# Optimization experiments

Hardware: AMD Instinct MI355X
Metric: run time of the kernel (lower is better)

## Reference

```python
import jax, jax.numpy as jnp
import numpy as np
import math

B, H, T, N = 2, 16, 4096, 64  # N = mlp_internal_dim_multiplier * n_embd // n_head = 1*1024//16
THETA = 2.0 ** 16


def _cos_sin(T, N):
    # quantized-theta RoPE tables, matching get_freqs + angle construction
    t = jnp.arange(N, dtype=jnp.float32)
    tq = jnp.floor(t / 2.0) * 2.0                      # quantize(t, q=2)
    freqs = 1.0 / (THETA ** (tq / N)) / (2.0 * math.pi)  # [N]
    phases = jnp.arange(T, dtype=jnp.float32)[:, None] * freqs[None, :]  # [T,N]
    ang = (phases % 1.0) * (2.0 * math.pi)
    return jnp.cos(ang), jnp.sin(ang)                  # each [T,N]


def setup_inputs() -> dict:
    key = jax.random.key(0)
    kq, kv = jax.random.split(key)
    Q = jax.random.normal(kq, (B, H, T, N), dtype=jnp.float32)
    V = jax.random.normal(kv, (B, H, T, N), dtype=jnp.float32)
    return {"Q": Q, "V": V}


def reference(Q, V):
    # K is Q (asserted in the torch module); RoPE applied to Q only.
    b, h, t, n = Q.shape
    cos, sin = _cos_sin(t, n)                          # [t,n], broadcast over b,h
    q_rot = jnp.stack((-Q[..., 1::2], Q[..., ::2]), axis=-1).reshape(Q.shape)
    QR = Q * cos + q_rot * sin                         # [b,h,t,n]
    scores = jnp.einsum('bhtn,bhsn->bhts', QR, QR) * (n ** -0.5)
    # strict lower-triangular mask (tril with diagonal=-1): no softmax
    mask = jnp.tril(jnp.ones((t, t), dtype=bool), k=-1)
    scores = jnp.where(mask, scores, 0.0)
    return jnp.einsum('bhts,bhsn->bhtn', scores, V)
```

## Files before the change

kernel.cpp:

```cpp
#include <hip/hip_runtime.h>

#define T_SEQ 4096
#define NDIM 64
#define BH 32
#define TN (T_SEQ * NDIM)

typedef short short8 __attribute__((ext_vector_type(8)));
typedef float f32x16 __attribute__((ext_vector_type(16)));
typedef unsigned uint2e __attribute__((ext_vector_type(2)));

static __device__ __forceinline__ unsigned packbf(float lo, float hi) {
    unsigned r;
    asm("v_cvt_pk_bf16_f32 %0, %1, %2" : "=v"(r) : "v"(lo), "v"(hi));
    return r;
}
static __device__ __forceinline__ unsigned short f2bf(float x) {
    union { float f; unsigned u; } v; v.f = x;
    return (unsigned short)((v.u + 0x8000u) >> 16);
}
static __device__ __forceinline__ f32x16 mfma32(short8 a, short8 b, f32x16 c) {
    return __builtin_amdgcn_mfma_f32_32x32x16_bf16(a, b, c, 0, 0, 0);
}

static __device__ __forceinline__ void half_swap(unsigned &x, unsigned &y) {
#if __has_builtin(__builtin_amdgcn_permlane32_swap)
    uint2e r = __builtin_amdgcn_permlane32_swap(x, y, false, false);
    x = r[0]; y = r[1];
#else
    int sl = (((int)threadIdx.x & 63) ^ 32) << 2;
    unsigned bx = (unsigned)__builtin_amdgcn_ds_bpermute(sl, (int)x);
    unsigned by = (unsigned)__builtin_amdgcn_ds_bpermute(sl, (int)y);
    bool hi = (threadIdx.x & 32) != 0;
    unsigned nx = hi ? by : x;
    unsigned ny = hi ? y : bx;
    x = nx; y = ny;
#endif
}

static __device__ __forceinline__ void tile_to_frags(const f32x16 &sc, short8 &f0, short8 &f1) {
    unsigned d[4][2];
#pragma unroll
    for (int g = 0; g < 4; ++g) {
        d[g][0] = packbf(sc[4 * g + 0], sc[4 * g + 1]);
        d[g][1] = packbf(sc[4 * g + 2], sc[4 * g + 3]);
    }
    half_swap(d[0][0], d[1][0]);
    half_swap(d[0][1], d[1][1]);
    half_swap(d[2][0], d[3][0]);
    half_swap(d[2][1], d[3][1]);
    union { unsigned u[4]; short8 s; } a, b;
    a.u[0] = d[0][0]; a.u[1] = d[0][1]; a.u[2] = d[1][0]; a.u[3] = d[1][1];
    b.u[0] = d[2][0]; b.u[1] = d[2][1]; b.u[2] = d[3][0]; b.u[3] = d[3][1];
    f0 = a.s; f1 = b.s;
}

__global__ __launch_bounds__(256) void rope_kernel(const float* __restrict__ Q,
                                                   unsigned short* __restrict__ qf) {
    const int bhtb = blockIdx.x;
    const int tb = bhtb & 127;
    const int bh = bhtb >> 7;
    const int np = threadIdx.x & 31;
    const int tg = threadIdx.x >> 5;
    const float freq = exp2f(-0.5f * (float)np) * 0.15915494309189535f;
    const int kc = np >> 3, hi = (np >> 2) & 1, jw = np & 3;
    const float2* qsrc = (const float2*)(Q + ((size_t)bh * T_SEQ + tb * 32) * NDIM);
    unsigned* qdst = (unsigned*)(qf + (size_t)bh * TN + (size_t)tb * 32 * NDIM);
#pragma unroll
    for (int it = 0; it < 4; ++it) {
        const int tl = tg * 4 + it;
        const int t = tb * 32 + tl;
        float2 q = qsrc[tl * 32 + np];
        float ph = (float)t * freq;
        float ang = (ph - floorf(ph)) * 6.283185307179586f;
        float s, c;
        __sincosf(ang, &s, &c);
        float r0 = q.x * c - q.y * s;
        float r1 = q.y * c + q.x * s;
        qdst[kc * 256 + (tl * 2 + hi) * 4 + jw] = packbf(r0, r1);
    }
}

__global__ __launch_bounds__(256) void vtrans_kernel(const float* __restrict__ V,
                                                     unsigned short* __restrict__ vfr) {
    __shared__ float tile[128 * 65];
    const int sb = blockIdx.x;
    const int bh = blockIdx.y;
    const int tid = threadIdx.x;
    const float* vsrc = V + ((size_t)bh * T_SEQ + sb * 128) * NDIM;
#pragma unroll
    for (int i = 0; i < 8; ++i) {
        int e = (i * 256 + tid) * 4;
        int row = e >> 6, col = e & 63;
        float4 d4 = *(const float4*)(vsrc + e);
        tile[row * 65 + col + 0] = d4.x; tile[row * 65 + col + 1] = d4.y;
        tile[row * 65 + col + 2] = d4.z; tile[row * 65 + col + 3] = d4.w;
    }
    __syncthreads();
    unsigned short* dst = vfr + (size_t)bh * TN + (size_t)sb * 8192;
#pragma unroll
    for (int u = 0; u < 4; ++u) {
        int g = u * 256 + tid;
        int kc = g >> 7, dh = g & 127;
        int d = dh >> 1, hh = dh & 1;
        int sbase = kc * 16 + hh * 8;
        uint4 o;
        o.x = packbf(tile[(sbase + 0) * 65 + d] * 0.125f, tile[(sbase + 1) * 65 + d] * 0.125f);
        o.y = packbf(tile[(sbase + 2) * 65 + d] * 0.125f, tile[(sbase + 3) * 65 + d] * 0.125f);
        o.z = packbf(tile[(sbase + 4) * 65 + d] * 0.125f, tile[(sbase + 5) * 65 + d] * 0.125f);
        o.w = packbf(tile[(sbase + 6) * 65 + d] * 0.125f, tile[(sbase + 7) * 65 + d] * 0.125f);
        *(uint4*)(dst + g * 8) = o;
    }
}

__global__ __launch_bounds__(256, 2) void attn_kernel(const unsigned short* __restrict__ qf,
                                                      const unsigned short* __restrict__ vfr,
                                                      float* __restrict__ out) {
    __shared__ float4 red[2][4][4][64];

    const int tid = threadIdx.x;
    const int lane = tid & 63;
    const int w = tid >> 6;
    const int ws = w >> 1, wt = w & 1;
    const int l31 = lane & 31, hi = lane >> 5;

    const int blk = blockIdx.x;
    const int bh = blk & 31;
    const int qb = 31 - (blk >> 5);
    const int t0 = qb * 128;

    const unsigned short* qfh = qf + (size_t)bh * TN;
    const unsigned short* vfh = vfr + (size_t)bh * TN;
    float* out_h = out + (size_t)bh * TN;

    const int lhx16 = (l31 * 2 + hi) * 8;

    short8 bq[2][4];
#pragma unroll
    for (int tt2 = 0; tt2 < 2; ++tt2) {
        const int r32 = (t0 >> 5) + 2 * wt + tt2;
#pragma unroll
        for (int kc = 0; kc < 4; ++kc)
            bq[tt2][kc] = *(const short8*)(qfh + (size_t)(r32 * 4 + kc) * 512 + lhx16);
    }

    f32x16 oacc[2][2];
#pragma unroll
    for (int a = 0; a < 2; ++a)
#pragma unroll
        for (int b = 0; b < 2; ++b)
#pragma unroll
            for (int r = 0; r < 16; ++r) oacc[a][b][r] = 0.0f;

    short8 ak[2][4];
#pragma unroll
    for (int st2 = 0; st2 < 2; ++st2) {
        const int r32 = 2 * ws + st2;
#pragma unroll
        for (int kc = 0; kc < 4; ++kc)
            ak[st2][kc] = *(const short8*)(qfh + (size_t)(r32 * 4 + kc) * 512 + lhx16);
    }

    for (int sb = 0; sb <= qb; ++sb) {
        f32x16 sacc[2][2];
#pragma unroll
        for (int a = 0; a < 2; ++a)
#pragma unroll
            for (int b = 0; b < 2; ++b)
#pragma unroll
                for (int r = 0; r < 16; ++r) sacc[a][b][r] = 0.0f;
#pragma unroll
        for (int st2 = 0; st2 < 2; ++st2)
#pragma unroll
            for (int tt2 = 0; tt2 < 2; ++tt2)
#pragma unroll
                for (int kc = 0; kc < 4; ++kc)
                    sacc[st2][tt2] = mfma32(ak[st2][kc], bq[tt2][kc], sacc[st2][tt2]);

        short8 akn[2][4];
        if (sb < qb) {
#pragma unroll
            for (int st2 = 0; st2 < 2; ++st2) {
                const int r32 = (sb + 1) * 4 + 2 * ws + st2;
#pragma unroll
                for (int kc = 0; kc < 4; ++kc)
                    akn[st2][kc] = *(const short8*)(qfh + (size_t)(r32 * 4 + kc) * 512 + lhx16);
            }
        }

        if (sb == qb) {
#pragma unroll
            for (int st2 = 0; st2 < 2; ++st2) {
                const int st = 2 * ws + st2;
#pragma unroll
                for (int tt2 = 0; tt2 < 2; ++tt2) {
                    const int tg = (2 * wt + tt2) * 32 + l31;
#pragma unroll
                    for (int r = 0; r < 16; ++r) {
                        const int sg = st * 32 + (r & 3) + 8 * (r >> 2) + 4 * hi;
                        if (sg >= tg) sacc[st2][tt2][r] = 0.0f;
                    }
                }
            }
        }

        short8 pa[2][4];
#pragma unroll
        for (int st2 = 0; st2 < 2; ++st2)
#pragma unroll
            for (int tt2 = 0; tt2 < 2; ++tt2)
                tile_to_frags(sacc[st2][tt2], pa[tt2][2 * st2 + 0], pa[tt2][2 * st2 + 1]);

#pragma unroll
        for (int kc4 = 0; kc4 < 4; ++kc4) {
            const int kcg = 4 * ws + kc4;
            short8 v0 = *(const short8*)(vfh + (size_t)sb * 8192 + (size_t)kcg * 1024 + lhx16);
            short8 v1 = *(const short8*)(vfh + (size_t)sb * 8192 + (size_t)kcg * 1024 + 512 + lhx16);
            oacc[0][0] = mfma32(pa[0][kc4], v0, oacc[0][0]);
            oacc[0][1] = mfma32(pa[0][kc4], v1, oacc[0][1]);
            oacc[1][0] = mfma32(pa[1][kc4], v0, oacc[1][0]);
            oacc[1][1] = mfma32(pa[1][kc4], v1, oacc[1][1]);
        }

        if (sb < qb) {
#pragma unroll
            for (int st2 = 0; st2 < 2; ++st2)
#pragma unroll
                for (int kc = 0; kc < 4; ++kc)
                    ak[st2][kc] = akn[st2][kc];
        }
    }

    if (ws == 1) {
#pragma unroll
        for (int tt2 = 0; tt2 < 2; ++tt2)
#pragma unroll
            for (int dd = 0; dd < 2; ++dd)
#pragma unroll
                for (int g = 0; g < 4; ++g) {
                    float4 v;
                    v.x = oacc[tt2][dd][4 * g + 0];
                    v.y = oacc[tt2][dd][4 * g + 1];
                    v.z = oacc[tt2][dd][4 * g + 2];
                    v.w = oacc[tt2][dd][4 * g + 3];
                    red[wt][tt2 * 2 + dd][g][lane] = v;
                }
    }
    __syncthreads();
    if (ws == 0) {
#pragma unroll
        for (int tt2 = 0; tt2 < 2; ++tt2)
#pragma unroll
            for (int dd = 0; dd < 2; ++dd) {
#pragma unroll
                for (int g = 0; g < 4; ++g) {
                    float4 o = red[wt][tt2 * 2 + dd][g][lane];
                    oacc[tt2][dd][4 * g + 0] += o.x;
                    oacc[tt2][dd][4 * g + 1] += o.y;
                    oacc[tt2][dd][4 * g + 2] += o.z;
                    oacc[tt2][dd][4 * g + 3] += o.w;
                }
#pragma unroll
                for (int r = 0; r < 16; ++r) {
                    const int rl = (r & 3) + 8 * (r >> 2) + 4 * hi;
                    out_h[(size_t)(t0 + 64 * wt + 32 * tt2 + rl) * NDIM + 32 * dd + l31] =
                        oacc[tt2][dd][r];
                }
            }
    }
    (void)f2bf(0.0f);
}

extern "C" void kernel_launch(void* const* d_in, const int* in_sizes, int n_in,
                              void* d_out, int out_size, void* d_ws, size_t ws_size,
                              hipStream_t stream) {
    (void)in_sizes; (void)n_in; (void)out_size; (void)ws_size;
    const float* Q = (const float*)d_in[0];
    const float* V = (const float*)d_in[1];
    float* out = (float*)d_out;

    unsigned short* qf  = (unsigned short*)d_ws;
    unsigned short* vfr = qf + (size_t)BH * TN;

    rope_kernel<<<BH * 128, 256, 0, stream>>>(Q, qf);
    vtrans_kernel<<<dim3(T_SEQ / 128, BH), 256, 0, stream>>>(V, vfr);
    attn_kernel<<<BH * 32, 256, 0, stream>>>(qf, vfr, out);
}
```

Measured before the change: 177.3 us.

## Split attention block across eight waves with per-tile diagonal skipping

Each block now runs 512 threads as eight waves. Every wave owns one 32-row query tile and half of each 128-key block, where before four waves each owned two query tiles. On the diagonal key block, waves skip key tiles that lie fully above the causal mask instead of computing and then zeroing them. The software prefetch of next-block keys is removed, and K and V fragments are loaded inline per tile. The intent is more wave parallelism, lower register pressure, higher occupancy and less wasted diagonal work, at the cost of more redundant Q/V loads per block and losing the explicit prefetch.

```diff
diff --git a/kernel.cpp b/kernel.cpp
--- a/kernel.cpp
+++ b/kernel.cpp
@@ -13,10 +13,6 @@
     unsigned r;
     asm("v_cvt_pk_bf16_f32 %0, %1, %2" : "=v"(r) : "v"(lo), "v"(hi));
     return r;
-}
-static __device__ __forceinline__ unsigned short f2bf(float x) {
-    union { float f; unsigned u; } v; v.f = x;
-    return (unsigned short)((v.u + 0x8000u) >> 16);
 }
 static __device__ __forceinline__ f32x16 mfma32(short8 a, short8 b, f32x16 c) {
     return __builtin_amdgcn_mfma_f32_32x32x16_bf16(a, b, c, 0, 0, 0);
@@ -112,15 +108,15 @@
     }
 }
 
-__global__ __launch_bounds__(256, 2) void attn_kernel(const unsigned short* __restrict__ qf,
+__global__ __launch_bounds__(512, 3) void attn_kernel(const unsigned short* __restrict__ qf,
                                                       const unsigned short* __restrict__ vfr,
                                                       float* __restrict__ out) {
-    __shared__ float4 red[2][4][4][64];
+    __shared__ float4 red[4][2][4][64];
 
     const int tid = threadIdx.x;
     const int lane = tid & 63;
     const int w = tid >> 6;
-    const int ws = w >> 1, wt = w & 1;
+    const int ws = w >> 2, wt = w & 3;
     const int l31 = lane & 31, hi = lane >> 5;
 
     const int blk = blockIdx.x;
@@ -134,140 +130,96 @@
 
     const int lhx16 = (l31 * 2 + hi) * 8;
 
-    short8 bq[2][4];
-#pragma unroll
-    for (int tt2 = 0; tt2 < 2; ++tt2) {
-        const int r32 = (t0 >> 5) + 2 * wt + tt2;
+    short8 bq[4];
+    {
+        const int tr32 = (t0 >> 5) + wt;
 #pragma unroll
         for (int kc = 0; kc < 4; ++kc)
-            bq[tt2][kc] = *(const short8*)(qfh + (size_t)(r32 * 4 + kc) * 512 + lhx16);
-    }
-
-    f32x16 oacc[2][2];
+            bq[kc] = *(const short8*)(qfh + (size_t)(tr32 * 4 + kc) * 512 + lhx16);
+    }
+
+    f32x16 oacc[2];
 #pragma unroll
     for (int a = 0; a < 2; ++a)
 #pragma unroll
-        for (int b = 0; b < 2; ++b)
-#pragma unroll
-            for (int r = 0; r < 16; ++r) oacc[a][b][r] = 0.0f;
-
-    short8 ak[2][4];
-#pragma unroll
-    for (int st2 = 0; st2 < 2; ++st2) {
-        const int r32 = 2 * ws + st2;
-#pragma unroll
-        for (int kc = 0; kc < 4; ++kc)
-            ak[st2][kc] = *(const short8*)(qfh + (size_t)(r32 * 4 + kc) * 512 + lhx16);
-    }
+        for (int r = 0; r < 16; ++r) oacc[a][r] = 0.0f;
 
     for (int sb = 0; sb <= qb; ++sb) {
-        f32x16 sacc[2][2];
-#pragma unroll
-        for (int a = 0; a < 2; ++a)
-#pragma unroll
-            for (int b = 0; b < 2; ++b)
-#pragma unroll
-                for (int r = 0; r < 16; ++r) sacc[a][b][r] = 0.0f;
-#pragma unroll
-        for (int st2 = 0; st2 < 2; ++st2)
-#pragma unroll
-            for (int tt2 = 0; tt2 < 2; ++tt2)
-#pragma unroll
-                for (int kc = 0; kc < 4; ++kc)
-                    sacc[st2][tt2] = mfma32(ak[st2][kc], bq[tt2][kc], sacc[st2][tt2]);
-
-        short8 akn[2][4];
-        if (sb < qb) {
-#pragma unroll
-            for (int st2 = 0; st2 < 2; ++st2) {
-                const int r32 = (sb + 1) * 4 + 2 * ws + st2;
-#pragma unroll
-                for (int kc = 0; kc < 4; ++kc)
-                    akn[st2][kc] = *(const short8*)(qfh + (size_t)(r32 * 4 + kc) * 512 + lhx16);
-            }
+        const bool diag = (sb == qb);
+#pragma unroll
+        for (int st2 = 0; st2 < 2; ++st2) {
+            const int idx = 2 * ws + st2;
+            if (diag && idx > wt) continue;
+
+            const int sr32 = sb * 4 + idx;
+            short8 vf00 = *(const short8*)(vfh + (size_t)sb * 8192 + (size_t)(2 * idx + 0) * 1024 + lhx16);
+            short8 vf01 = *(const short8*)(vfh + (size_t)sb * 8192 + (size_t)(2 * idx + 0) * 1024 + 512 + lhx16);
+            short8 vf10 = *(const short8*)(vfh + (size_t)sb * 8192 + (size_t)(2 * idx + 1) * 1024 + lhx16);
+            short8 vf11 = *(const short8*)(vfh + (size_t)sb * 8192 + (size_t)(2 * idx + 1) * 1024 + 512 + lhx16);
+
+            short8 ak[4];
+#pragma unroll
+            for (int kc = 0; kc < 4; ++kc)
+                ak[kc] = *(const short8*)(qfh + (size_t)(sr32 * 4 + kc) * 512 + lhx16);
+
+            f32x16 sacc;
+#pragma unroll
+            for (int r = 0; r < 16; ++r) sacc[r] = 0.0f;
+#pragma unroll
+            for (int kc = 0; kc < 4; ++kc)
+                sacc = mfma32(ak[kc], bq[kc], sacc);
+
+            if (diag && idx == wt) {
+                const int tg = l31;
+#pragma unroll
+                for (int r = 0; r < 16; ++r) {
+                    const int sg = (r & 3) + 8 * (r >> 2) + 4 * hi;
+                    if (sg >= tg) sacc[r] = 0.0f;
+                }
+            }
+
+            short8 p0, p1;
+            tile_to_frags(sacc, p0, p1);
+
+            oacc[0] = mfma32(p0, vf00, oacc[0]);
+            oacc[1] = mfma32(p0, vf01, oacc[1]);
+            oacc[0] = mfma32(p1, vf10, oacc[0]);
+            oacc[1] = mfma32(p1, vf11, oacc[1]);
         }
-
-        if (sb == qb) {
-#pragma unroll
-            for (int st2 = 0; st2 < 2; ++st2) {
-                const int st = 2 * ws + st2;
-#pragma unroll
-                for (int tt2 = 0; tt2 < 2; ++tt2) {
-                    const int tg = (2 * wt + tt2) * 32 + l31;
-#pragma unroll
-                    for (int r = 0; r < 16; ++r) {
-                        const int sg = st * 32 + (r & 3) + 8 * (r >> 2) + 4 * hi;
-                        if (sg >= tg) sacc[st2][tt2][r] = 0.0f;
-                    }
-                }
-            }
-        }
-
-        short8 pa[2][4];
-#pragma unroll
-        for (int st2 = 0; st2 < 2; ++st2)
-#pragma unroll
-            for (int tt2 = 0; tt2 < 2; ++tt2)
-                tile_to_frags(sacc[st2][tt2], pa[tt2][2 * st2 + 0], pa[tt2][2 * st2 + 1]);
-
-#pragma unroll
-        for (int kc4 = 0; kc4 < 4; ++kc4) {
-            const int kcg = 4 * ws + kc4;
-            short8 v0 = *(const short8*)(vfh + (size_t)sb * 8192 + (size_t)kcg * 1024 + lhx16);
-            short8 v1 = *(const short8*)(vfh + (size_t)sb * 8192 + (size_t)kcg * 1024 + 512 + lhx16);
-            oacc[0][0] = mfma32(pa[0][kc4], v0, oacc[0][0]);
-            oacc[0][1] = mfma32(pa[0][kc4], v1, oacc[0][1]);
-            oacc[1][0] = mfma32(pa[1][kc4], v0, oacc[1][0]);
-            oacc[1][1] = mfma32(pa[1][kc4], v1, oacc[1][1]);
-        }
-
-        if (sb < qb) {
-#pragma unroll
-            for (int st2 = 0; st2 < 2; ++st2)
-#pragma unroll
-                for (int kc = 0; kc < 4; ++kc)
-                    ak[st2][kc] = akn[st2][kc];
-        }
     }
 
     if (ws == 1) {
 #pragma unroll
-        for (int tt2 = 0; tt2 < 2; ++tt2)
-#pragma unroll
-            for (int dd = 0; dd < 2; ++dd)
-#pragma unroll
-                for (int g = 0; g < 4; ++g) {
-                    float4 v;
-                    v.x = oacc[tt2][dd][4 * g + 0];
-                    v.y = oacc[tt2][dd][4 * g + 1];
-                    v.z = oacc[tt2][dd][4 * g + 2];
-                    v.w = oacc[tt2][dd][4 * g + 3];
-                    red[wt][tt2 * 2 + dd][g][lane] = v;
-                }
+        for (int dd = 0; dd < 2; ++dd)
+#pragma unroll
+            for (int g = 0; g < 4; ++g) {
+                float4 v;
+                v.x = oacc[dd][4 * g + 0];
+                v.y = oacc[dd][4 * g + 1];
+                v.z = oacc[dd][4 * g + 2];
+                v.w = oacc[dd][4 * g + 3];
+                red[wt][dd][g][lane] = v;
+            }
     }
     __syncthreads();
     if (ws == 0) {
 #pragma unroll
-        for (int tt2 = 0; tt2 < 2; ++tt2)
-#pragma unroll
-            for (int dd = 0; dd < 2; ++dd) {
-#pragma unroll
-                for (int g = 0; g < 4; ++g) {
-                    float4 o = red[wt][tt2 * 2 + dd][g][lane];
-                    oacc[tt2][dd][4 * g + 0] += o.x;
-                    oacc[tt2][dd][4 * g + 1] += o.y;
-                    oacc[tt2][dd][4 * g + 2] += o.z;
-                    oacc[tt2][dd][4 * g + 3] += o.w;
-                }
-#pragma unroll
-                for (int r = 0; r < 16; ++r) {
-                    const int rl = (r & 3) + 8 * (r >> 2) + 4 * hi;
-                    out_h[(size_t)(t0 + 64 * wt + 32 * tt2 + rl) * NDIM + 32 * dd + l31] =
-                        oacc[tt2][dd][r];
-                }
-            }
-    }
-    (void)f2bf(0.0f);
+        for (int dd = 0; dd < 2; ++dd) {
+#pragma unroll
+            for (int g = 0; g < 4; ++g) {
+                float4 o = red[wt][dd][g][lane];
+                oacc[dd][4 * g + 0] += o.x;
+                oacc[dd][4 * g + 1] += o.y;
+                oacc[dd][4 * g + 2] += o.z;
+                oacc[dd][4 * g + 3] += o.w;
+            }
+#pragma unroll
+            for (int r = 0; r < 16; ++r) {
+                const int rl = (r & 3) + 8 * (r >> 2) + 4 * hi;
+                out_h[(size_t)(t0 + 32 * wt + rl) * NDIM + 32 * dd + l31] = oacc[dd][r];
+            }
+        }
+    }
 }
 
 extern "C" void kernel_launch(void* const* d_in, const int* in_sizes, int n_in,
@@ -283,5 +235,5 @@
 
     rope_kernel<<<BH * 128, 256, 0, stream>>>(Q, qf);
     vtrans_kernel<<<dim3(T_SEQ / 128, BH), 256, 0, stream>>>(V, vfr);
-    attn_kernel<<<BH * 32, 256, 0, stream>>>(qf, vfr, out);
-}
+    attn_kernel<<<BH * 32, 512, 0, stream>>>(qf, vfr, out);
+}
```

Result: no change. 180.8 us (+2.0%).

## Software-pipeline attention loop: overlap next S-phase MFMAs with current O-phase

Applied to the files above, without the earlier changes.

Restructures the attention main loop into a software pipeline. Iteration sb now converts scores sb to bf16 fragments, computes scores for block sb+1, runs the O-phase MFMAs for block sb, and prefetches K two blocks ahead and V one block ahead into registers. The diagonal mask now runs only once, in an epilogue after the loop. The goal is to hide global-load latency and the dependency stalls between the score MFMAs, the fragment transform and the output MFMAs, at the cost of more live registers (V fragments plus the score accumulators), which could raise spills under launch_bounds(256,2).

```diff
diff --git a/kernel.cpp b/kernel.cpp
--- a/kernel.cpp
+++ b/kernel.cpp
@@ -13,10 +13,6 @@
     unsigned r;
     asm("v_cvt_pk_bf16_f32 %0, %1, %2" : "=v"(r) : "v"(lo), "v"(hi));
     return r;
-}
-static __device__ __forceinline__ unsigned short f2bf(float x) {
-    union { float f; unsigned u; } v; v.f = x;
-    return (unsigned short)((v.u + 0x8000u) >> 16);
 }
 static __device__ __forceinline__ f32x16 mfma32(short8 a, short8 b, f32x16 c) {
     return __builtin_amdgcn_mfma_f32_32x32x16_bf16(a, b, c, 0, 0, 0);
@@ -112,6 +108,58 @@
     }
 }
 
+static __device__ __forceinline__ void load_ak4(const unsigned short* qfh, int sb, int ws,
+                                                int lhx16, short8 (&A)[2][4]) {
+    const int r32base = sb * 4 + 2 * ws;
+#pragma unroll
+    for (int st2 = 0; st2 < 2; ++st2)
+#pragma unroll
+        for (int kc = 0; kc < 4; ++kc)
+            A[st2][kc] = *(const short8*)(qfh + (size_t)((r32base + st2) * 4 + kc) * 512 + lhx16);
+}
+static __device__ __forceinline__ void load_vf8(const unsigned short* vfh, int sb, int ws,
+                                                int lhx16, short8 (&V)[4][2]) {
+#pragma unroll
+    for (int kc4 = 0; kc4 < 4; ++kc4) {
+        const size_t base = (size_t)sb * 8192 + (size_t)(4 * ws + kc4) * 1024 + lhx16;
+        V[kc4][0] = *(const short8*)(vfh + base);
+        V[kc4][1] = *(const short8*)(vfh + base + 512);
+    }
+}
+static __device__ __forceinline__ void s_phase(const short8 (&ak)[2][4], const short8 (&bq)[2][4],
+                                               f32x16 (&sacc)[2][2]) {
+#pragma unroll
+    for (int a = 0; a < 2; ++a)
+#pragma unroll
+        for (int b = 0; b < 2; ++b)
+#pragma unroll
+            for (int r = 0; r < 16; ++r) sacc[a][b][r] = 0.0f;
+#pragma unroll
+    for (int st2 = 0; st2 < 2; ++st2)
+#pragma unroll
+        for (int tt2 = 0; tt2 < 2; ++tt2)
+#pragma unroll
+            for (int kc = 0; kc < 4; ++kc)
+                sacc[st2][tt2] = mfma32(ak[st2][kc], bq[tt2][kc], sacc[st2][tt2]);
+}
+static __device__ __forceinline__ void transform_all(const f32x16 (&sacc)[2][2], short8 (&pa)[2][4]) {
+#pragma unroll
+    for (int st2 = 0; st2 < 2; ++st2)
+#pragma unroll
+        for (int tt2 = 0; tt2 < 2; ++tt2)
+            tile_to_frags(sacc[st2][tt2], pa[tt2][2 * st2 + 0], pa[tt2][2 * st2 + 1]);
+}
+static __device__ __forceinline__ void o_phase(const short8 (&pa)[2][4], const short8 (&vf)[4][2],
+                                               f32x16 (&oacc)[2][2]) {
+#pragma unroll
+    for (int kc4 = 0; kc4 < 4; ++kc4) {
+        oacc[0][0] = mfma32(pa[0][kc4], vf[kc4][0], oacc[0][0]);
+        oacc[0][1] = mfma32(pa[0][kc4], vf[kc4][1], oacc[0][1]);
+        oacc[1][0] = mfma32(pa[1][kc4], vf[kc4][0], oacc[1][0]);
+        oacc[1][1] = mfma32(pa[1][kc4], vf[kc4][1], oacc[1][1]);
+    }
+}
+
 __global__ __launch_bounds__(256, 2) void attn_kernel(const unsigned short* __restrict__ qf,
                                                       const unsigned short* __restrict__ vfr,
                                                       float* __restrict__ out) {
@@ -151,83 +199,40 @@
 #pragma unroll
             for (int r = 0; r < 16; ++r) oacc[a][b][r] = 0.0f;
 
-    short8 ak[2][4];
-#pragma unroll
-    for (int st2 = 0; st2 < 2; ++st2) {
-        const int r32 = 2 * ws + st2;
-#pragma unroll
-        for (int kc = 0; kc < 4; ++kc)
-            ak[st2][kc] = *(const short8*)(qfh + (size_t)(r32 * 4 + kc) * 512 + lhx16);
-    }
-
-    for (int sb = 0; sb <= qb; ++sb) {
-        f32x16 sacc[2][2];
-#pragma unroll
-        for (int a = 0; a < 2; ++a)
-#pragma unroll
-            for (int b = 0; b < 2; ++b)
-#pragma unroll
-                for (int r = 0; r < 16; ++r) sacc[a][b][r] = 0.0f;
-#pragma unroll
-        for (int st2 = 0; st2 < 2; ++st2)
-#pragma unroll
-            for (int tt2 = 0; tt2 < 2; ++tt2)
-#pragma unroll
-                for (int kc = 0; kc < 4; ++kc)
-                    sacc[st2][tt2] = mfma32(ak[st2][kc], bq[tt2][kc], sacc[st2][tt2]);
-
-        short8 akn[2][4];
-        if (sb < qb) {
-#pragma unroll
-            for (int st2 = 0; st2 < 2; ++st2) {
-                const int r32 = (sb + 1) * 4 + 2 * ws + st2;
-#pragma unroll
-                for (int kc = 0; kc < 4; ++kc)
-                    akn[st2][kc] = *(const short8*)(qfh + (size_t)(r32 * 4 + kc) * 512 + lhx16);
+    short8 ak[2][4], vf[4][2];
+    f32x16 sacc[2][2];
+    load_ak4(qfh, 0, ws, lhx16, ak);
+    load_vf8(vfh, 0, ws, lhx16, vf);
+    s_phase(ak, bq, sacc);
+    load_ak4(qfh, (1 <= qb ? 1 : qb), ws, lhx16, ak);
+
+    for (int sb = 0; sb < qb; ++sb) {
+        short8 pa[2][4];
+        transform_all(sacc, pa);
+        s_phase(ak, bq, sacc);
+        o_phase(pa, vf, oacc);
+        const int nak = (sb + 2 <= qb) ? sb + 2 : qb;
+        load_ak4(qfh, nak, ws, lhx16, ak);
+        load_vf8(vfh, sb + 1, ws, lhx16, vf);
+    }
+
+    {
+#pragma unroll
+        for (int st2 = 0; st2 < 2; ++st2) {
+            const int st = 2 * ws + st2;
+#pragma unroll
+            for (int tt2 = 0; tt2 < 2; ++tt2) {
+                const int tg = (2 * wt + tt2) * 32 + l31;
+#pragma unroll
+                for (int r = 0; r < 16; ++r) {
+                    const int sg = st * 32 + (r & 3) + 8 * (r >> 2) + 4 * hi;
+                    if (sg >= tg) sacc[st2][tt2][r] = 0.0f;
+                }
             }
         }
-
-        if (sb == qb) {
-#pragma unroll
-            for (int st2 = 0; st2 < 2; ++st2) {
-                const int st = 2 * ws + st2;
-#pragma unroll
-                for (int tt2 = 0; tt2 < 2; ++tt2) {
-                    const int tg = (2 * wt + tt2) * 32 + l31;
-#pragma unroll
-                    for (int r = 0; r < 16; ++r) {
-                        const int sg = st * 32 + (r & 3) + 8 * (r >> 2) + 4 * hi;
-                        if (sg >= tg) sacc[st2][tt2][r] = 0.0f;
-                    }
-                }
-            }
-        }
-
         short8 pa[2][4];
-#pragma unroll
-        for (int st2 = 0; st2 < 2; ++st2)
-#pragma unroll
-            for (int tt2 = 0; tt2 < 2; ++tt2)
-                tile_to_frags(sacc[st2][tt2], pa[tt2][2 * st2 + 0], pa[tt2][2 * st2 + 1]);
-
-#pragma unroll
-        for (int kc4 = 0; kc4 < 4; ++kc4) {
-            const int kcg = 4 * ws + kc4;
-            short8 v0 = *(const short8*)(vfh + (size_t)sb * 8192 + (size_t)kcg * 1024 + lhx16);
-            short8 v1 = *(const short8*)(vfh + (size_t)sb * 8192 + (size_t)kcg * 1024 + 512 + lhx16);
-            oacc[0][0] = mfma32(pa[0][kc4], v0, oacc[0][0]);
-            oacc[0][1] = mfma32(pa[0][kc4], v1, oacc[0][1]);
-            oacc[1][0] = mfma32(pa[1][kc4], v0, oacc[1][0]);
-            oacc[1][1] = mfma32(pa[1][kc4], v1, oacc[1][1]);
-        }
-
-        if (sb < qb) {
-#pragma unroll
-            for (int st2 = 0; st2 < 2; ++st2)
-#pragma unroll
-                for (int kc = 0; kc < 4; ++kc)
-                    ak[st2][kc] = akn[st2][kc];
-        }
+        transform_all(sacc, pa);
+        o_phase(pa, vf, oacc);
     }
 
     if (ws == 1) {
@@ -267,7 +272,6 @@
                 }
             }
     }
-    (void)f2bf(0.0f);
 }
 
 extern "C" void kernel_launch(void* const* d_in, const int* in_sizes, int n_in,
```

New measurement: 174.2 us. About the same (-1.7%).
